# Performance work log

Measured on AMD Instinct MI355X. Metric: run time of the kernel, lower is better.

Reference implementation:

```python
import jax, jax.numpy as jnp
import numpy as np

ALPHA, BETA, LAMB, GAMMA = 1.0, 1.0, 1e-4, 1.0
K_NN, TAU = 50, 0.1
EPS = 1e-8


def _sqdist(A, B):
    # ||a - b||^2, clamped at 0 like the torch code
    d2 = (A * A).sum(1)[:, None] + (B * B).sum(1)[None, :] - 2.0 * (A @ B.T)
    return jnp.maximum(d2, 0.0)


def _mmd(s, t):
    comb = jnp.concatenate([s, t], axis=0)
    sigma_sq = jax.lax.stop_gradient(jnp.median(_sqdist(comb, comb))) / 2.0
    sigma_sq = jnp.where(sigma_sq < 1e-6, jnp.float32(1.0), sigma_sq)
    g = 1.0 / (sigma_sq + EPS)
    kxx = jnp.exp(-g * _sqdist(s, s)).mean()
    kyy = jnp.exp(-g * _sqdist(t, t)).mean()
    kxy = jnp.exp(-g * _sqdist(s, t)).mean()
    return jnp.maximum(kxx + kyy - 2.0 * kxy, 0.0)


def setup_inputs() -> dict:
    key = jax.random.key(0)
    ks = jax.random.split(key, 8)
    B, d, N, Nq, K = 256, 128, 200000, 10000, K_NN
    q_batch = jax.random.normal(ks[0], (B, d), jnp.float32)
    X = jax.random.normal(ks[1], (N, d), jnp.float32)
    W = jax.random.normal(ks[2], (d, d), jnp.float32) * (1.0 / np.sqrt(d))
    b = jnp.zeros((d,), jnp.float32)
    pre_weights = jax.random.uniform(ks[3], (Nq, K), jnp.float32)
    pre_weights = pre_weights / pre_weights.sum(1, keepdims=True)
    pre_indices = jax.random.randint(ks[4], (Nq, K), 0, N)
    q_indices = jax.random.randint(ks[5], (B,), 0, Nq)
    idx = jax.random.randint(ks[6], (B,), 0, N)
    return {"q_batch": q_batch, "X": X, "W": W, "b": b,
            "pre_weights": pre_weights, "pre_indices": pre_indices,
            "q_indices": q_indices, "idx": idx}


def reference(q_batch, X, W, b, pre_weights, pre_indices, q_indices, idx):
    Tq = q_batch @ W.T + b                                   # model(q_batch), Linear(d, d)
    # ---- MMD between mapped queries and a random database batch ----
    loss_dist = _mmd(Tq, X[idx])
    # ---- exact KNN (faiss IndexFlatL2 equivalent) on detached embeddings ----
    d2_all = _sqdist(jax.lax.stop_gradient(Tq), X)           # [B, N]
    _, post_idx = jax.lax.top_k(-d2_all, K_NN)               # [B, K] nearest neighbors
    Xn = X[post_idx]                                         # [B, K, d]
    l2 = ((Tq[:, None, :] - Xn) ** 2).sum(-1)                # [B, K] (grad flows here)
    post_w = jax.nn.softmax(-l2 / TAU, axis=1)
    # ---- union-KL, vectorized over batch (exact torch.unique semantics) ----
    pre_i = pre_indices[q_indices]                           # [B, K]
    pre_w = pre_weights[q_indices]                           # [B, K]
    cat = jnp.concatenate([pre_i, post_idx], axis=1)         # [B, 2K]
    # multiplicity of each id within the concatenated list -> collapse duplicates
    mult = (cat[:, :, None] == cat[:, None, :]).sum(-1).astype(jnp.float32)  # [B, 2K]
    p_raw = jnp.einsum('bmk,bk->bm',
                       (cat[:, :, None] == pre_i[:, None, :]).astype(jnp.float32), pre_w)
    q_raw = jnp.einsum('bmk,bk->bm',
                       (cat[:, :, None] == post_idx[:, None, :]).astype(jnp.float32), post_w)
    p_c = jnp.maximum(p_raw, EPS)
    q_c = jnp.maximum(q_raw, EPS)
    p = p_c / (p_c / mult).sum(1, keepdims=True)             # normalize over union
    q = q_c / (q_c / mult).sum(1, keepdims=True)
    kl = ((p * (jnp.log(p) - jnp.log(q))) / mult).sum(1)     # KL(p || q) per sample
    loss_knn = kl.mean()
    # ---- L2 regularization of model params & anchor loss ----
    loss_reg = 0.5 * ((W ** 2).sum() + (b ** 2).sum())
    loss_anchor = ((Tq - q_batch) ** 2).sum(1).mean()
    total = ALPHA * loss_dist + BETA * loss_knn + LAMB * loss_reg + GAMMA * loss_anchor
    return jnp.stack([total, loss_dist, loss_knn, loss_anchor])
```

## Files before the change

kernel.cpp:

```cpp
#include <hip/hip_runtime.h>
#include <cstdint>

#define D 128
#define NPTS 200000
#define KNN 50
#define CAP 8192
#define NS 8192
#define SLACK 2.0f
#define EB 2048

#define OFF_ACC    0
#define OFF_SEL    256
#define OFF_CNT    1024
#define OFF_HIST0  17408
#define OFF_HIST12 148480
#define ZERO_BYTES 214016
#define OFF_COMB   214016
#define OFF_D2     476160
#define OFF_XN     1524736
#define OFF_SAMP   2324736
#define OFF_EBUF   2324736
#define OFF_THR    10713344
#define OFF_CANDI  10714368
#define OFF_KSG    19102976
#define OFF_BCNT   19102976
#define OFF_TQSW   27491584
#define OFF_XBF    27557120
#define OFF_ANCP   78757120
#define OFF_WREGP  78758144

typedef __attribute__((ext_vector_type(8))) short bf16x8;
typedef __attribute__((ext_vector_type(4))) float f32x4;
typedef const __attribute__((address_space(1))) void* gas_p;
typedef __attribute__((address_space(3))) void* las_p;

__device__ __forceinline__ unsigned fkey(float f) {
    unsigned u = __float_as_uint(f);
    return u ^ ((unsigned)((int)u >> 31) | 0x80000000u);
}

__device__ __forceinline__ void stage8k(const unsigned short* __restrict__ g,
                                        unsigned short* l, int w, int lane)
{
    #pragma unroll
    for (int j = 0; j < 2; j++) {
        const unsigned short* gp = g + j * 2048 + w * 512 + lane * 8;
        unsigned short* lp = l + j * 2048 + w * 512;
        __builtin_amdgcn_global_load_lds((gas_p)gp, (las_p)lp, 16, 0, 0);
    }
}

__global__ void k_phase1(const float* __restrict__ q, const float* __restrict__ X,
                         const float* __restrict__ W, const float* __restrict__ bb,
                         const int* __restrict__ idx, float* __restrict__ comb,
                         unsigned short* __restrict__ tqsw, unsigned short* __restrict__ xbf,
                         float* __restrict__ xn, float* __restrict__ ancp,
                         float* __restrict__ wregp, float* __restrict__ wszero)
{
    const int blk = blockIdx.x, t = threadIdx.x;
    if (blk < 12500) {
        __shared__ float xr4[4][16];
        const int lr = t & 15;
        const float4* src = (const float4*)(X + ((long)(blk * 16 + lr)) * D + (t >> 4) * 8);
        float4 v0 = src[0], v1 = src[1];
        uint4 pk;
        pk.x = (__float_as_uint(v0.x) >> 16) | (__float_as_uint(v0.y) & 0xFFFF0000u);
        pk.y = (__float_as_uint(v0.z) >> 16) | (__float_as_uint(v0.w) & 0xFFFF0000u);
        pk.z = (__float_as_uint(v1.x) >> 16) | (__float_as_uint(v1.y) & 0xFFFF0000u);
        pk.w = (__float_as_uint(v1.z) >> 16) | (__float_as_uint(v1.w) & 0xFFFF0000u);
        *(uint4*)(xbf + (long)blk * 2048 + t * 8) = pk;
        float ssq = v0.x*v0.x + v0.y*v0.y + v0.z*v0.z + v0.w*v0.w
                  + v1.x*v1.x + v1.y*v1.y + v1.z*v1.z + v1.w*v1.w;
        ssq += __shfl_down(ssq, 32);
        ssq += __shfl_down(ssq, 16);
        if ((t & 63) < 16) xr4[t >> 6][lr] = ssq;
        __syncthreads();
        if (t < 16) xn[blk * 16 + t] = xr4[0][t] + xr4[1][t] + xr4[2][t] + xr4[3][t];
    } else if (blk < 12628) {
        __shared__ float rowv[2][D];
        __shared__ float red[2][D];
        const int half = t >> 7, tt = t & 127;
        const int row = (blk - 12500) * 2 + half;
        rowv[half][tt] = q[row * D + tt];
        __syncthreads();
        float s = 0.f;
        const float* wr = W + tt * D;
        #pragma unroll 4
        for (int k = 0; k < D; k++) s = fmaf(rowv[half][k], wr[k], s);
        s += bb[tt];
        comb[row * D + tt] = s;
        unsigned ub = __float_as_uint(s);
        unsigned short hv = (unsigned short)((ub + 0x7fffu + ((ub >> 16) & 1u)) >> 16);
        int ksb = tt >> 5, quad = (tt & 31) >> 3, jj = tt & 7;
        int lane = quad * 16 + (row & 15);
        tqsw[(row >> 4) * 2048 + ksb * 512 + lane * 8 + jj] = hv;
        float dd = s - rowv[half][tt];
        red[half][tt] = dd * dd;
        __syncthreads();
        for (int off = 64; off > 0; off >>= 1) { if (tt < off) red[half][tt] += red[half][tt + off]; __syncthreads(); }
        if (tt == 0) ancp[row] = red[half][0];
    } else if (blk < 12756) {
        const int half = t >> 7, tt = t & 127;
        const int i = (blk - 12628) * 2 + half;
        comb[(256 + i) * D + tt] = X[(long)idx[i] * D + tt];
    } else if (blk < 12760) {
        __shared__ float wred[4];
        const int base = (blk - 12756) * 4096;
        float s = 0.f;
        #pragma unroll 4
        for (int k = 0; k < 16; k++) { float v = W[base + k * 256 + t]; s = fmaf(v, v, s); }
        if (blk == 12756 && t < D) { float v = bb[t]; s = fmaf(v, v, s); }
        #pragma unroll
        for (int off = 32; off > 0; off >>= 1) s += __shfl_down(s, off);
        if ((t & 63) == 0) wred[t >> 6] = s;
        __syncthreads();
        if (t == 0) wregp[blk - 12756] = wred[0] + wred[1] + wred[2] + wred[3];
    } else {
        uint4* z = (uint4*)wszero;
        const uint4 zz = make_uint4(0u, 0u, 0u, 0u);
        for (int i = (blk - 12760) * 256 + t; i < (ZERO_BYTES / 16); i += 1024) z[i] = zz;
    }
}

__global__ void k_d2m(const float* __restrict__ comb, float* __restrict__ D2w,
                      unsigned* __restrict__ hist0, const unsigned short* __restrict__ tqsw,
                      const unsigned short* __restrict__ xbf, const float* __restrict__ xn,
                      float* __restrict__ samp)
{
    __shared__ __align__(16) char smraw[51456];
    const int b = blockIdx.x, t = threadIdx.x;
    if (b < 1024) {
        float (*cj)[D + 1] = (float(*)[D + 1])smraw;
        float (*ci)[D]     = (float(*)[D])(smraw + 33024);
        unsigned* h        = (unsigned*)(smraw + 35072);
        const int ib = b >> 3, jb = b & 7;
        const int w = t >> 6, l = t & 63;
        for (int m = t; m < 4096; m += 256) h[m] = 0;
        const int irow = ib * 4 + w;
        ci[w][l] = comb[irow * D + l];
        ci[w][l + 64] = comb[irow * D + l + 64];
        const float4* src = (const float4*)(comb + (jb * 64) * D);
        #pragma unroll
        for (int m = 0; m < 8; m++) {
            int u = m * 256 + t;
            int r = u >> 5, c = u & 31;
            float4 v = src[u];
            cj[r][c * 4 + 0] = v.x; cj[r][c * 4 + 1] = v.y; cj[r][c * 4 + 2] = v.z; cj[r][c * 4 + 3] = v.w;
        }
        __syncthreads();
        float s = 0.f;
        #pragma unroll 4
        for (int k = 0; k < D; k++) { float d = ci[w][k] - cj[l][k]; s = fmaf(d, d, s); }
        D2w[irow * 512 + jb * 64 + l] = s;
        atomicAdd(&h[__float_as_uint(s) >> 20], 1u);
        __syncthreads();
        const int sh = (ib + jb) & 7;
        for (int m = t; m < 4096; m += 256) { unsigned v = h[m]; if (v) atomicAdd(&hist0[m * 8 + sh], v); }
    } else {
        unsigned short* sb = (unsigned short*)smraw;
        const int w = t >> 6, lane = t & 63;
        const int lr = lane & 15, quad = lane >> 4;
        const int ck = b - 1024;
        stage8k(xbf + (long)ck * 4096, sb, w, lane);
        bf16x8 a[4][4];
        #pragma unroll
        for (int i = 0; i < 4; i++)
            #pragma unroll
            for (int ks = 0; ks < 4; ks++)
                a[i][ks] = *(const bf16x8*)(tqsw + (w * 4 + i) * 2048 + ks * 512 + lane * 8);
        __syncthreads();
        #pragma unroll
        for (int tt = 0; tt < 2; tt++) {
            const int r = (ck * 2 + tt) * 16 + lr;
            float xnv = xn[r];
            bf16x8 bfr[4];
            #pragma unroll
            for (int ks = 0; ks < 4; ks++)
                bfr[ks] = *(const bf16x8*)(sb + tt * 2048 + ks * 512 + lane * 8);
            f32x4 acc4[4];
            #pragma unroll
            for (int i = 0; i < 4; i++) acc4[i] = (f32x4){0.f, 0.f, 0.f, 0.f};
            #pragma unroll
            for (int ks = 0; ks < 4; ks++)
                #pragma unroll
                for (int i = 0; i < 4; i++)
                    acc4[i] = __builtin_amdgcn_mfma_f32_16x16x32_bf16(a[i][ks], bfr[ks], acc4[i], 0, 0, 0);
            #pragma unroll
            for (int i = 0; i < 4; i++)
                #pragma unroll
                for (int reg = 0; reg < 4; reg++) {
                    int qq = w * 64 + i * 16 + quad * 4 + reg;
                    samp[qq * NS + r] = xnv - 2.f * acc4[i][reg];
                }
        }
    }
}

__global__ void k_h1thr(const float* __restrict__ D2w, unsigned* __restrict__ hist12,
                        const unsigned* __restrict__ hist0, unsigned* __restrict__ sel,
                        const float* __restrict__ samp, float* __restrict__ thr)
{
    __shared__ unsigned buf[8192];
    __shared__ unsigned bins[4096];
    __shared__ unsigned part[256];
    __shared__ unsigned selll[4];
    __shared__ unsigned wred[4];
    const int t = threadIdx.x;
    if (blockIdx.x < 256) {
        unsigned s = 0;
        #pragma unroll
        for (int m = 0; m < 16; m++) {
            int bin = t * 16 + m;
            unsigned bs = 0;
            #pragma unroll
            for (int sh = 0; sh < 8; sh++) bs += hist0[bin * 8 + sh];
            bins[bin] = bs;
            s += bs;
        }
        part[t] = s;
        for (int m = t; m < 8192; m += 256) buf[m] = 0;
        __syncthreads();
        if (t == 0) {
            for (int tg = 0; tg < 2; tg++) {
                unsigned r = tg ? 131072u : 131071u;
                int c = 0;
                while (part[c] <= r) { r -= part[c]; c++; }
                int b = c * 16;
                while (bins[b] <= r) { r -= bins[b]; b++; }
                selll[2 * tg] = (unsigned)b; selll[2 * tg + 1] = r;
            }
            if (blockIdx.x == 0) {
                sel[0] = selll[0]; sel[1] = selll[1]; sel[2] = selll[2]; sel[3] = selll[3];
            }
        }
        __syncthreads();
        unsigned p0 = selll[0], p1 = selll[2];
        const int e0 = blockIdx.x * 1024;
        for (int m = 0; m < 4; m++) {
            unsigned key = __float_as_uint(D2w[e0 + m * 256 + t]);
            if ((key >> 20) == p0) atomicAdd(&buf[(key >> 8) & 0xFFFu], 1u);
            if ((key >> 20) == p1) atomicAdd(&buf[4096 + ((key >> 8) & 0xFFFu)], 1u);
        }
        __syncthreads();
        for (int m = t; m < 8192; m += 256) { unsigned v = buf[m]; if (v) atomicAdd(&hist12[m], v); }
    } else {
        const int q = blockIdx.x - 256;
        unsigned kreg[32];
        #pragma unroll
        for (int i = 0; i < 32; i++) kreg[i] = fkey(samp[q * NS + i * 256 + t]);
        unsigned v = 0;
        for (int bit = 31; bit >= 0; bit--) {
            unsigned trial = v | (1u << bit);
            unsigned c = 0;
            #pragma unroll
            for (int i = 0; i < 32; i++) c += (kreg[i] < trial) ? 1u : 0u;
            #pragma unroll
            for (int off = 32; off > 0; off >>= 1) c += __shfl_down(c, off);
            if ((t & 63) == 0) wred[t >> 6] = c;
            __syncthreads();
            unsigned total = wred[0] + wred[1] + wred[2] + wred[3];
            __syncthreads();
            if (total <= (unsigned)(KNN - 1)) v = trial;
        }
        if (t == 0) {
            unsigned orig = (v & 0x80000000u) ? (v ^ 0x80000000u) : ~v;
            thr[q] = __uint_as_float(orig) + SLACK;
        }
    }
}

__global__ __launch_bounds__(256) void k_filt2(const unsigned short* __restrict__ tqsw,
    const unsigned short* __restrict__ xbf, const float* __restrict__ xn,
    const float* __restrict__ thr, unsigned* __restrict__ ebuf, unsigned* __restrict__ bcnt,
    const float* __restrict__ D2w, unsigned* __restrict__ hist12,
    unsigned* __restrict__ sel)
{
    if (blockIdx.x >= 1024) {
        __shared__ unsigned h2c[512];
        __shared__ unsigned part2[256];
        __shared__ unsigned pfx[2];
        __shared__ unsigned rr[2];
        const int t = threadIdx.x;
        for (int tg = 0; tg < 2; tg++) {
            const unsigned* hh = hist12 + tg * 4096;
            unsigned s = 0;
            for (int m = 0; m < 16; m++) s += hh[t * 16 + m];
            part2[t] = s;
            __syncthreads();
            if (t == 0) {
                unsigned r = sel[1 + 2 * tg];
                int c = 0;
                while (part2[c] <= r) { r -= part2[c]; c++; }
                int b = c * 16;
                while (hh[b] <= r) { r -= hh[b]; b++; }
                pfx[tg] = (sel[2 * tg] << 12) | (unsigned)b;
                rr[tg] = r;
            }
            __syncthreads();
        }
        if (blockIdx.x == 1024 && t == 0) {
            sel[4] = pfx[0]; sel[5] = rr[0]; sel[6] = pfx[1]; sel[7] = rr[1];
        }
        h2c[t] = 0; h2c[256 + t] = 0;
        __syncthreads();
        unsigned p0 = pfx[0], p1 = pfx[1];
        const int e0 = (blockIdx.x - 1024) * 1024;
        for (int m = 0; m < 4; m++) {
            unsigned key = __float_as_uint(D2w[e0 + m * 256 + t]);
            if ((key >> 8) == p0) atomicAdd(&h2c[key & 0xFFu], 1u);
            if ((key >> 8) == p1) atomicAdd(&h2c[256 + (key & 0xFFu)], 1u);
        }
        __syncthreads();
        unsigned* gp = hist12 + 8192;
        unsigned v0 = h2c[t], v1 = h2c[256 + t];
        if (v0) atomicAdd(&gp[t], v0);
        if (v1) atomicAdd(&gp[4096 + t], v1);
        return;
    }
    __shared__ unsigned short sb[2][4096];
    __shared__ unsigned lbuf[1024];
    __shared__ unsigned lcnt;
    __shared__ unsigned gbase;
    const int t = threadIdx.x;
    const int w = t >> 6, lane = t & 63;
    const int lr = lane & 15, quad = lane >> 4;
    unsigned* eb = ebuf + (unsigned)blockIdx.x * EB;
    bf16x8 a[4][4];
    #pragma unroll
    for (int i = 0; i < 4; i++)
        #pragma unroll
        for (int ks = 0; ks < 4; ks++)
            a[i][ks] = *(const bf16x8*)(tqsw + (w * 4 + i) * 2048 + ks * 512 + lane * 8);
    float th_r[4][4];
    #pragma unroll
    for (int i = 0; i < 4; i++)
        #pragma unroll
        for (int reg = 0; reg < 4; reg++)
            th_r[i][reg] = thr[w * 64 + i * 16 + quad * 4 + reg];
    int ck = blockIdx.x;
    int cur = 0;
    if (t == 0) { lcnt = 0; gbase = 0; }
    stage8k(xbf + (long)ck * 4096, sb[0], w, lane);
    __syncthreads();
    while (true) {
        const int ckn = ck + 1024;
        const bool has = ckn < 6250;
        if (has) stage8k(xbf + (long)ckn * 4096, sb[cur ^ 1], w, lane);
        #pragma unroll
        for (int tt = 0; tt < 2; tt++) {
            const int r = (ck * 2 + tt) * 16 + lr;
            float xnv = xn[r];
            bf16x8 b[4];
            #pragma unroll
            for (int ks = 0; ks < 4; ks++)
                b[ks] = *(const bf16x8*)(sb[cur] + tt * 2048 + ks * 512 + lane * 8);
            f32x4 acc4[4];
            #pragma unroll
            for (int i = 0; i < 4; i++) acc4[i] = (f32x4){0.f, 0.f, 0.f, 0.f};
            #pragma unroll
            for (int ks = 0; ks < 4; ks++)
                #pragma unroll
                for (int i = 0; i < 4; i++)
                    acc4[i] = __builtin_amdgcn_mfma_f32_16x16x32_bf16(a[i][ks], b[ks], acc4[i], 0, 0, 0);
            #pragma unroll
            for (int i = 0; i < 4; i++)
                #pragma unroll
                for (int reg = 0; reg < 4; reg++) {
                    float s = xnv - 2.f * acc4[i][reg];
                    if (s <= th_r[i][reg]) {
                        unsigned qq = (unsigned)(w * 64 + i * 16 + quad * 4 + reg);
                        unsigned p = atomicAdd(&lcnt, 1u);
                        if (p < 1024u) lbuf[p] = (qq << 18) | (unsigned)r;
                        else {
                            unsigned d = gbase + p;
                            if (d < EB) eb[d] = (qq << 18) | (unsigned)r;
                        }
                    }
                }
        }
        __syncthreads();
        unsigned n = lcnt;
        if (!has || n >= 512u) {
            unsigned nf = (n < 1024u) ? n : 1024u;
            unsigned gb = gbase;
            for (unsigned m = t; m < nf; m += 256) {
                unsigned d = gb + m;
                if (d < EB) eb[d] = lbuf[m];
            }
            __syncthreads();
            if (t == 0) { gbase = gb + n; lcnt = 0; }
            __syncthreads();
        }
        if (!has) break;
        ck = ckn; cur ^= 1;
    }
    if (t == 0) bcnt[blockIdx.x] = (gbase < EB) ? gbase : EB;
}

__global__ __launch_bounds__(256) void k_scatmmd(const unsigned* __restrict__ ebuf,
    const unsigned* __restrict__ bcnt, int* __restrict__ cand_i, unsigned* __restrict__ cnt,
    const float* __restrict__ D2w, const unsigned* __restrict__ hist12,
    const unsigned* __restrict__ sel, float* __restrict__ acc)
{
    const int t = threadIdx.x;
    if (blockIdx.x >= 128) {
        __shared__ unsigned h2[512];
        __shared__ float gsh;
        __shared__ float part[12];
        const int w = t >> 6;
        h2[t] = hist12[8192 + t];
        h2[256 + t] = hist12[8192 + 4096 + t];
        __syncthreads();
        if (t == 0) {
            unsigned key[2];
            for (int tg = 0; tg < 2; tg++) {
                unsigned r = sel[5 + 2 * tg];
                const unsigned* hh = h2 + tg * 256;
                int b = 0;
                while (hh[b] <= r) { r -= hh[b]; b++; }
                key[tg] = (sel[4 + 2 * tg] << 8) | (unsigned)b;
            }
            float med = 0.5f * (__uint_as_float(key[0]) + __uint_as_float(key[1]));
            float ssq = 0.5f * med;
            if (ssq < 1e-6f) ssq = 1.0f;
            gsh = 1.0f / (ssq + 1e-8f);
        }
        __syncthreads();
        const float g = gsh;
        float s[3] = {0.f, 0.f, 0.f};
        const int e0 = (blockIdx.x - 128) * 1024;
        #pragma unroll
        for (int m = 0; m < 4; m++) {
            int e = e0 + m * 256 + t;
            int i = e >> 9, j = e & 511;
            float v = expf(-g * D2w[e]);
            int qd = (i < 256) ? ((j < 256) ? 0 : 2) : ((j < 256) ? 2 : 1);
            s[qd] += v;
        }
        #pragma unroll
        for (int c = 0; c < 3; c++) {
            float x = s[c];
            #pragma unroll
            for (int off = 32; off > 0; off >>= 1) x += __shfl_down(x, off);
            if ((t & 63) == 0) part[w * 3 + c] = x;
        }
        __syncthreads();
        if (t == 0)
            for (int c = 0; c < 3; c++)
                atomicAdd(&acc[2 + c], part[c] + part[3 + c] + part[6 + c] + part[9 + c]);
        return;
    }
    __shared__ unsigned hist[256];
    __shared__ unsigned startp[256];
    const int b0 = blockIdx.x * 8;
    hist[t] = 0;
    __syncthreads();
    for (int b = b0; b < b0 + 8; b++) {
        unsigned n = bcnt[b];
        const unsigned* e = ebuf + (unsigned)b * EB;
        for (unsigned m = t; m < n; m += 256)
            atomicAdd(&hist[e[m] >> 18], 1u);
    }
    __syncthreads();
    unsigned c = hist[t];
    if (c) {
        unsigned base = atomicAdd(&cnt[t * 16], c);
        startp[t] = ((unsigned)t << 13) + base;
    }
    __syncthreads();
    for (int b = b0; b < b0 + 8; b++) {
        unsigned n = bcnt[b];
        const unsigned* e = ebuf + (unsigned)b * EB;
        for (unsigned m = t; m < n; m += 256) {
            unsigned ent = e[m];
            unsigned qq = ent >> 18;
            unsigned pos = atomicAdd(&startp[qq], 1u);
            if (pos < ((qq + 1u) << 13)) cand_i[pos] = (int)(ent & 0x3FFFFu);
        }
    }
}

__global__ void k_rescore(const float* __restrict__ comb, const float* __restrict__ X,
                          const float* __restrict__ xn, const int* __restrict__ cand_i,
                          const unsigned* __restrict__ cnt, unsigned* __restrict__ ksg)
{
    __shared__ float qrow[D];
    const int q = blockIdx.x, sp = blockIdx.y, t = threadIdx.x;
    if (t < D) qrow[t] = comb[q * D + t];
    __syncthreads();
    unsigned nn = cnt[q * 16];
    const int n = (nn < (unsigned)CAP) ? (int)nn : CAP;
    const int g = t >> 3, j = t & 7;
    for (int m = sp * 32 + g; m < n; m += 512) {
        int r = cand_i[q * CAP + m];
        const float4* xr = (const float4*)(X + (long)r * D);
        float s = 0.f;
        #pragma unroll
        for (int p = 0; p < 4; p++) {
            float4 xv = xr[j * 4 + p];
            float4 qv = *(const float4*)&qrow[(j * 4 + p) * 4];
            s = fmaf(xv.x, qv.x, fmaf(xv.y, qv.y, fmaf(xv.z, qv.z, fmaf(xv.w, qv.w, s))));
        }
        s += __shfl_down(s, 4); s += __shfl_down(s, 2); s += __shfl_down(s, 1);
        if (j == 0) ksg[q * CAP + m] = fkey(xn[r] - 2.f * s);
    }
}

__global__ void k_post2(const float* __restrict__ comb, const float* __restrict__ X,
                        const int* __restrict__ cand_i, const unsigned* __restrict__ cnt,
                        const unsigned* __restrict__ ksg, const int* __restrict__ pri,
                        const float* __restrict__ prw, const int* __restrict__ qix,
                        float* __restrict__ acc, unsigned* __restrict__ sel,
                        const float* __restrict__ ancp, const float* __restrict__ wregp,
                        float* __restrict__ out)
{
    __shared__ unsigned ks[CAP];
    __shared__ float qrow[D];
    __shared__ unsigned wred[4];
    __shared__ unsigned wpos, eqn;
    __shared__ int eq[64];
    __shared__ int pidx[KNN];
    __shared__ float l2s[KNN];
    __shared__ float pw[KNN];
    __shared__ int ci[100];
    __shared__ float pwv[50], qwv[50];
    __shared__ float pterm[100], qterm[100], kterm[100];
    __shared__ float Sp, Sq;
    const int q = blockIdx.x, t = threadIdx.x;
    if (t < D) qrow[t] = comb[q * D + t];
    if (t == 0) { wpos = 0; eqn = 0; }
    unsigned nn = cnt[q * 16];
    const int n = (nn < (unsigned)CAP) ? (int)nn : CAP;
    for (int m = t; m < n; m += 256) ks[m] = ksg[q * CAP + m];
    __syncthreads();
    int kk = KNN - 1; if (kk > n - 1) kk = n - 1;
    unsigned v = 0;
    for (int bit = 31; bit >= 0; bit--) {
        unsigned trial = v | (1u << bit);
        unsigned c = 0;
        for (int m = t; m < n; m += 256) c += (ks[m] < trial) ? 1u : 0u;
        #pragma unroll
        for (int off = 32; off > 0; off >>= 1) c += __shfl_down(c, off);
        if ((t & 63) == 0) wred[t >> 6] = c;
        __syncthreads();
        unsigned total = wred[0] + wred[1] + wred[2] + wred[3];
        __syncthreads();
        if (total <= (unsigned)kk) v = trial;
    }
    for (int m = t; m < n; m += 256) {
        if (ks[m] < v) {
            unsigned p = atomicAdd(&wpos, 1u);
            pidx[p] = cand_i[q * CAP + m];
        } else if (ks[m] == v) {
            unsigned p = atomicAdd(&eqn, 1u);
            if (p < 64) eq[p] = cand_i[q * CAP + m];
        }
    }
    __syncthreads();
    if (t == 0) {
        int c1 = (int)wpos, need = KNN - c1;
        int ne = (eqn < 64u) ? (int)eqn : 64;
        for (int a = 0; a < ne; a++)
            for (int b2 = a + 1; b2 < ne; b2++)
                if (eq[b2] < eq[a]) { int tmp = eq[a]; eq[a] = eq[b2]; eq[b2] = tmp; }
        for (int a = 0; a < need && a < ne; a++) pidx[c1 + a] = eq[a];
    }
    __syncthreads();
    const int g = t >> 3, j = t & 7;
    for (int nb = g; nb < KNN; nb += 32) {
        long r = pidx[nb];
        const float4* xr = (const float4*)(X + r * D);
        float s = 0.f;
        #pragma unroll
        for (int p = 0; p < 4; p++) {
            float4 xv = xr[j * 4 + p];
            float4 qv = *(const float4*)&qrow[(j * 4 + p) * 4];
            float d0 = qv.x - xv.x, d1 = qv.y - xv.y, d2 = qv.z - xv.z, d3 = qv.w - xv.w;
            s += d0 * d0 + d1 * d1 + d2 * d2 + d3 * d3;
        }
        s += __shfl_down(s, 4); s += __shfl_down(s, 2); s += __shfl_down(s, 1);
        if (j == 0) l2s[nb] = s;
    }
    int qi = qix[q];
    if (t >= 128 && t < 178) { int k = t - 128; ci[k] = pri[qi * 50 + k]; pwv[k] = prw[qi * 50 + k]; }
    __syncthreads();
    if (t < 64) {
        float logit = (t < KNN) ? (-l2s[t] * 10.0f) : -3.4e38f;
        float m = logit;
        #pragma unroll
        for (int off = 32; off > 0; off >>= 1) m = fmaxf(m, __shfl_down(m, off));
        m = __shfl(m, 0);
        float e = (t < KNN) ? expf(logit - m) : 0.f;
        float ss = e;
        #pragma unroll
        for (int off = 32; off > 0; off >>= 1) ss += __shfl_down(ss, off);
        ss = __shfl(ss, 0);
        if (t < KNN) pw[t] = e / ss;
    }
    __syncthreads();
    if (t < 50) { ci[50 + t] = pidx[t]; qwv[t] = pw[t]; }
    __syncthreads();
    float pc = 0.f, qc = 0.f, mult = 0.f;
    if (t < 100) {
        int c = ci[t];
        float pr = 0.f, qr = 0.f;
        for (int k = 0; k < 50; k++) {
            bool m1 = (c == ci[k]); bool m2 = (c == ci[50 + k]);
            mult += (m1 ? 1.f : 0.f) + (m2 ? 1.f : 0.f);
            pr += m1 ? pwv[k] : 0.f;
            qr += m2 ? qwv[k] : 0.f;
        }
        pc = fmaxf(pr, 1e-8f); qc = fmaxf(qr, 1e-8f);
        pterm[t] = pc / mult; qterm[t] = qc / mult;
    }
    __syncthreads();
    if (t == 0) { float a = 0.f, b2 = 0.f; for (int m = 0; m < 100; m++) { a += pterm[m]; b2 += qterm[m]; } Sp = a; Sq = b2; }
    __syncthreads();
    if (t < 100) {
        float p = pc / Sp, qq2 = qc / Sq;
        kterm[t] = (p * (logf(p) - logf(qq2))) / mult;
    }
    __syncthreads();
    if (t == 0) {
        float s = 0.f;
        for (int m = 0; m < 100; m++) s += kterm[m];
        atomicAdd(&acc[1], s);
        __threadfence();
        unsigned old = atomicAdd(&sel[15], 1u);
        if (old == 255u) {
            __threadfence();
            float lknn = atomicAdd(&acc[1], 0.f) / 256.f;
            float reg = 0.f;
            #pragma unroll
            for (int m = 0; m < 4; m++) reg += wregp[m];
            reg *= 0.5f;
            float anc = 0.f;
            for (int m = 0; m < 256; m++) anc += ancp[m];
            float lanc = anc / 256.f;
            float kxx = acc[2] / 65536.f, kyy = acc[3] / 65536.f, kxy = acc[4] / 131072.f;
            float ld = fmaxf(kxx + kyy - 2.f * kxy, 0.f);
            out[0] = ld + lknn + 1e-4f * reg + lanc;
            out[1] = ld; out[2] = lknn; out[3] = lanc;
        }
    }
}

extern "C" void kernel_launch(void* const* d_in, const int* in_sizes, int n_in,
                              void* d_out, int out_size, void* d_ws, size_t ws_size,
                              hipStream_t stream)
{
    (void)in_sizes; (void)n_in; (void)out_size; (void)ws_size;
    const float* q   = (const float*)d_in[0];
    const float* X   = (const float*)d_in[1];
    const float* W   = (const float*)d_in[2];
    const float* bb  = (const float*)d_in[3];
    const float* prw = (const float*)d_in[4];
    const int*   pri = (const int*)d_in[5];
    const int*   qix = (const int*)d_in[6];
    const int*   idx = (const int*)d_in[7];
    float* out = (float*)d_out;
    char* ws = (char*)d_ws;
    float*    acc   = (float*)(ws + OFF_ACC);
    unsigned* sel   = (unsigned*)(ws + OFF_SEL);
    unsigned* cnt   = (unsigned*)(ws + OFF_CNT);
    unsigned* hist0 = (unsigned*)(ws + OFF_HIST0);
    unsigned* hist12= (unsigned*)(ws + OFF_HIST12);
    float*    comb  = (float*)(ws + OFF_COMB);
    float*    D2w   = (float*)(ws + OFF_D2);
    float*    xn    = (float*)(ws + OFF_XN);
    float*    samp  = (float*)(ws + OFF_SAMP);
    float*    thr   = (float*)(ws + OFF_THR);
    int*      cix   = (int*)(ws + OFF_CANDI);
    unsigned* ksg   = (unsigned*)(ws + OFF_KSG);
    unsigned* ebuf  = (unsigned*)(ws + OFF_EBUF);
    unsigned* bcnt  = (unsigned*)(ws + OFF_BCNT);
    unsigned short* tqsw = (unsigned short*)(ws + OFF_TQSW);
    unsigned short* xbf  = (unsigned short*)(ws + OFF_XBF);
    float*    ancp  = (float*)(ws + OFF_ANCP);
    float*    wregp = (float*)(ws + OFF_WREGP);

    hipLaunchKernelGGL(k_phase1,  dim3(12764),   dim3(256), 0, stream, q, X, W, bb, idx, comb, tqsw, xbf, xn, ancp, wregp, acc);
    hipLaunchKernelGGL(k_d2m,     dim3(1280),    dim3(256), 0, stream, comb, D2w, hist0, tqsw, xbf, xn, samp);
    hipLaunchKernelGGL(k_h1thr,   dim3(512),     dim3(256), 0, stream, D2w, hist12, hist0, sel, samp, thr);
    hipLaunchKernelGGL(k_filt2,   dim3(1280),    dim3(256), 0, stream, tqsw, xbf, xn, thr, ebuf, bcnt, D2w, hist12, sel);
    hipLaunchKernelGGL(k_scatmmd, dim3(384),     dim3(256), 0, stream, ebuf, bcnt, cix, cnt, D2w, hist12, sel, acc);
    hipLaunchKernelGGL(k_rescore, dim3(256, 16), dim3(256), 0, stream, comb, X, xn, cix, cnt, ksg);
    hipLaunchKernelGGL(k_post2,   dim3(256),     dim3(256), 0, stream, comb, X, cix, cnt, ksg, pri, prw, qix, acc, sel, ancp, wregp, out);
}
```

Measured before the change: 366.3 us.

## Fuse rescore into post kernel with 1024 threads and split LDS double buffer

Merges the candidate rescoring kernel into the final post-processing kernel. The fused kernel uses 1024-thread blocks and writes the rescored keys straight into shared memory instead of a global buffer, which removes one launch and the round trip of the key array. It also holds keys in registers for the radix select. The filter kernel's double buffer becomes two named LDS arrays selected by an explicit phase branch, so buffer addresses are static. The cost is that rescoring now runs on only 256 blocks instead of 4096, which reduces the parallelism available for the gather over X.

```diff
diff --git a/kernel.cpp b/kernel.cpp
--- a/kernel.cpp
+++ b/kernel.cpp
@@ -22,7 +22,6 @@
 #define OFF_EBUF   2324736
 #define OFF_THR    10713344
 #define OFF_CANDI  10714368
-#define OFF_KSG    19102976
 #define OFF_BCNT   19102976
 #define OFF_TQSW   27491584
 #define OFF_XBF    27557120
@@ -268,6 +267,42 @@
         }
     }
 }
+
+#define FILT_BODY(SBUF)                                                              \
+    do {                                                                             \
+        _Pragma("unroll")                                                            \
+        for (int tt = 0; tt < 2; tt++) {                                             \
+            const int r = (ck * 2 + tt) * 16 + lr;                                   \
+            float xnv = xn[r];                                                       \
+            bf16x8 bv[4];                                                            \
+            _Pragma("unroll")                                                        \
+            for (int ks2 = 0; ks2 < 4; ks2++)                                        \
+                bv[ks2] = *(const bf16x8*)(SBUF + tt * 2048 + ks2 * 512 + lane * 8); \
+            f32x4 acc4[4];                                                           \
+            _Pragma("unroll")                                                        \
+            for (int i = 0; i < 4; i++) acc4[i] = (f32x4){0.f, 0.f, 0.f, 0.f};       \
+            _Pragma("unroll")                                                        \
+            for (int ks2 = 0; ks2 < 4; ks2++)                                        \
+                _Pragma("unroll")                                                    \
+                for (int i = 0; i < 4; i++)                                          \
+                    acc4[i] = __builtin_amdgcn_mfma_f32_16x16x32_bf16(a[i][ks2], bv[ks2], acc4[i], 0, 0, 0); \
+            _Pragma("unroll")                                                        \
+            for (int i = 0; i < 4; i++)                                              \
+                _Pragma("unroll")                                                    \
+                for (int reg = 0; reg < 4; reg++) {                                  \
+                    float s = xnv - 2.f * acc4[i][reg];                              \
+                    if (s <= th_r[i][reg]) {                                         \
+                        unsigned qq = (unsigned)(w * 64 + i * 16 + quad * 4 + reg);  \
+                        unsigned p = atomicAdd(&lcnt, 1u);                           \
+                        if (p < 1024u) lbuf[p] = (qq << 18) | (unsigned)r;           \
+                        else {                                                       \
+                            unsigned dd2 = gbase + p;                                \
+                            if (dd2 < EB) eb[dd2] = (qq << 18) | (unsigned)r;        \
+                        }                                                            \
+                    }                                                                \
+                }                                                                    \
+        }                                                                            \
+    } while (0)
 
 __global__ __launch_bounds__(256) void k_filt2(const unsigned short* __restrict__ tqsw,
     const unsigned short* __restrict__ xbf, const float* __restrict__ xn,
@@ -317,7 +352,8 @@
         if (v1) atomicAdd(&gp[4096 + t], v1);
         return;
     }
-    __shared__ unsigned short sb[2][4096];
+    __shared__ unsigned short sbA[4096];
+    __shared__ unsigned short sbB[4096];
     __shared__ unsigned lbuf[1024];
     __shared__ unsigned lcnt;
     __shared__ unsigned gbase;
@@ -338,45 +374,19 @@
         for (int reg = 0; reg < 4; reg++)
             th_r[i][reg] = thr[w * 64 + i * 16 + quad * 4 + reg];
     int ck = blockIdx.x;
-    int cur = 0;
+    bool phaseA = true;
     if (t == 0) { lcnt = 0; gbase = 0; }
-    stage8k(xbf + (long)ck * 4096, sb[0], w, lane);
+    stage8k(xbf + (long)ck * 4096, sbA, w, lane);
     __syncthreads();
     while (true) {
         const int ckn = ck + 1024;
         const bool has = ckn < 6250;
-        if (has) stage8k(xbf + (long)ckn * 4096, sb[cur ^ 1], w, lane);
-        #pragma unroll
-        for (int tt = 0; tt < 2; tt++) {
-            const int r = (ck * 2 + tt) * 16 + lr;
-            float xnv = xn[r];
-            bf16x8 b[4];
-            #pragma unroll
-            for (int ks = 0; ks < 4; ks++)
-                b[ks] = *(const bf16x8*)(sb[cur] + tt * 2048 + ks * 512 + lane * 8);
-            f32x4 acc4[4];
-            #pragma unroll
-            for (int i = 0; i < 4; i++) acc4[i] = (f32x4){0.f, 0.f, 0.f, 0.f};
-            #pragma unroll
-            for (int ks = 0; ks < 4; ks++)
-                #pragma unroll
-                for (int i = 0; i < 4; i++)
-                    acc4[i] = __builtin_amdgcn_mfma_f32_16x16x32_bf16(a[i][ks], b[ks], acc4[i], 0, 0, 0);
-            #pragma unroll
-            for (int i = 0; i < 4; i++)
-                #pragma unroll
-                for (int reg = 0; reg < 4; reg++) {
-                    float s = xnv - 2.f * acc4[i][reg];
-                    if (s <= th_r[i][reg]) {
-                        unsigned qq = (unsigned)(w * 64 + i * 16 + quad * 4 + reg);
-                        unsigned p = atomicAdd(&lcnt, 1u);
-                        if (p < 1024u) lbuf[p] = (qq << 18) | (unsigned)r;
-                        else {
-                            unsigned d = gbase + p;
-                            if (d < EB) eb[d] = (qq << 18) | (unsigned)r;
-                        }
-                    }
-                }
+        if (phaseA) {
+            if (has) stage8k(xbf + (long)ckn * 4096, sbB, w, lane);
+            FILT_BODY(sbA);
+        } else {
+            if (has) stage8k(xbf + (long)ckn * 4096, sbA, w, lane);
+            FILT_BODY(sbB);
         }
         __syncthreads();
         unsigned n = lcnt;
@@ -392,7 +402,7 @@
             __syncthreads();
         }
         if (!has) break;
-        ck = ckn; cur ^= 1;
+        ck = ckn; phaseA = !phaseA;
     }
     if (t == 0) bcnt[blockIdx.x] = (gbase < EB) ? gbase : EB;
 }
@@ -480,43 +490,19 @@
     }
 }
 
-__global__ void k_rescore(const float* __restrict__ comb, const float* __restrict__ X,
-                          const float* __restrict__ xn, const int* __restrict__ cand_i,
-                          const unsigned* __restrict__ cnt, unsigned* __restrict__ ksg)
-{
-    __shared__ float qrow[D];
-    const int q = blockIdx.x, sp = blockIdx.y, t = threadIdx.x;
-    if (t < D) qrow[t] = comb[q * D + t];
-    __syncthreads();
-    unsigned nn = cnt[q * 16];
-    const int n = (nn < (unsigned)CAP) ? (int)nn : CAP;
-    const int g = t >> 3, j = t & 7;
-    for (int m = sp * 32 + g; m < n; m += 512) {
-        int r = cand_i[q * CAP + m];
-        const float4* xr = (const float4*)(X + (long)r * D);
-        float s = 0.f;
-        #pragma unroll
-        for (int p = 0; p < 4; p++) {
-            float4 xv = xr[j * 4 + p];
-            float4 qv = *(const float4*)&qrow[(j * 4 + p) * 4];
-            s = fmaf(xv.x, qv.x, fmaf(xv.y, qv.y, fmaf(xv.z, qv.z, fmaf(xv.w, qv.w, s))));
-        }
-        s += __shfl_down(s, 4); s += __shfl_down(s, 2); s += __shfl_down(s, 1);
-        if (j == 0) ksg[q * CAP + m] = fkey(xn[r] - 2.f * s);
-    }
-}
-
-__global__ void k_post2(const float* __restrict__ comb, const float* __restrict__ X,
+__global__ __launch_bounds__(1024) void k_rp(const float* __restrict__ comb,
+                        const float* __restrict__ X,
                         const int* __restrict__ cand_i, const unsigned* __restrict__ cnt,
-                        const unsigned* __restrict__ ksg, const int* __restrict__ pri,
+                        const int* __restrict__ pri,
                         const float* __restrict__ prw, const int* __restrict__ qix,
+                        const float* __restrict__ xn,
                         float* __restrict__ acc, unsigned* __restrict__ sel,
                         const float* __restrict__ ancp, const float* __restrict__ wregp,
                         float* __restrict__ out)
 {
     __shared__ unsigned ks[CAP];
     __shared__ float qrow[D];
-    __shared__ unsigned wred[4];
+    __shared__ unsigned wred[16];
     __shared__ unsigned wpos, eqn;
     __shared__ int eq[64];
     __shared__ int pidx[KNN];
@@ -531,23 +517,46 @@
     if (t == 0) { wpos = 0; eqn = 0; }
     unsigned nn = cnt[q * 16];
     const int n = (nn < (unsigned)CAP) ? (int)nn : CAP;
-    for (int m = t; m < n; m += 256) ks[m] = ksg[q * CAP + m];
-    __syncthreads();
+    __syncthreads();
+    const int g = t >> 3, j = t & 7;
+    for (int m = g; m < n; m += 128) {
+        int r = cand_i[q * CAP + m];
+        const float4* xr = (const float4*)(X + (long)r * D);
+        float s = 0.f;
+        #pragma unroll
+        for (int p = 0; p < 4; p++) {
+            float4 xv = xr[j * 4 + p];
+            float4 qv = *(const float4*)&qrow[(j * 4 + p) * 4];
+            s = fmaf(xv.x, qv.x, fmaf(xv.y, qv.y, fmaf(xv.z, qv.z, fmaf(xv.w, qv.w, s))));
+        }
+        s += __shfl_down(s, 4); s += __shfl_down(s, 2); s += __shfl_down(s, 1);
+        if (j == 0) ks[m] = fkey(xn[r] - 2.f * s);
+    }
+    __syncthreads();
+    unsigned kreg[8];
+    #pragma unroll
+    for (int i = 0; i < 8; i++) {
+        int m = i * 1024 + t;
+        kreg[i] = (m < n) ? ks[m] : 0xFFFFFFFFu;
+    }
     int kk = KNN - 1; if (kk > n - 1) kk = n - 1;
     unsigned v = 0;
     for (int bit = 31; bit >= 0; bit--) {
         unsigned trial = v | (1u << bit);
         unsigned c = 0;
-        for (int m = t; m < n; m += 256) c += (ks[m] < trial) ? 1u : 0u;
+        #pragma unroll
+        for (int i = 0; i < 8; i++) c += (kreg[i] < trial) ? 1u : 0u;
         #pragma unroll
         for (int off = 32; off > 0; off >>= 1) c += __shfl_down(c, off);
         if ((t & 63) == 0) wred[t >> 6] = c;
         __syncthreads();
-        unsigned total = wred[0] + wred[1] + wred[2] + wred[3];
+        unsigned total = 0;
+        #pragma unroll
+        for (int i = 0; i < 16; i++) total += wred[i];
         __syncthreads();
         if (total <= (unsigned)kk) v = trial;
     }
-    for (int m = t; m < n; m += 256) {
+    for (int m = t; m < n; m += 1024) {
         if (ks[m] < v) {
             unsigned p = atomicAdd(&wpos, 1u);
             pidx[p] = cand_i[q * CAP + m];
@@ -566,8 +575,7 @@
         for (int a = 0; a < need && a < ne; a++) pidx[c1 + a] = eq[a];
     }
     __syncthreads();
-    const int g = t >> 3, j = t & 7;
-    for (int nb = g; nb < KNN; nb += 32) {
+    for (int nb = g; nb < KNN; nb += 128) {
         long r = pidx[nb];
         const float4* xr = (const float4*)(X + r * D);
         float s = 0.f;
@@ -671,7 +679,6 @@
     float*    samp  = (float*)(ws + OFF_SAMP);
     float*    thr   = (float*)(ws + OFF_THR);
     int*      cix   = (int*)(ws + OFF_CANDI);
-    unsigned* ksg   = (unsigned*)(ws + OFF_KSG);
     unsigned* ebuf  = (unsigned*)(ws + OFF_EBUF);
     unsigned* bcnt  = (unsigned*)(ws + OFF_BCNT);
     unsigned short* tqsw = (unsigned short*)(ws + OFF_TQSW);
@@ -684,6 +691,5 @@
     hipLaunchKernelGGL(k_h1thr,   dim3(512),     dim3(256), 0, stream, D2w, hist12, hist0, sel, samp, thr);
     hipLaunchKernelGGL(k_filt2,   dim3(1280),    dim3(256), 0, stream, tqsw, xbf, xn, thr, ebuf, bcnt, D2w, hist12, sel);
     hipLaunchKernelGGL(k_scatmmd, dim3(384),     dim3(256), 0, stream, ebuf, bcnt, cix, cnt, D2w, hist12, sel, acc);
-    hipLaunchKernelGGL(k_rescore, dim3(256, 16), dim3(256), 0, stream, comb, X, xn, cix, cnt, ksg);
-    hipLaunchKernelGGL(k_post2,   dim3(256),     dim3(256), 0, stream, comb, X, cix, cnt, ksg, pri, prw, qix, acc, sel, ancp, wregp, out);
-}
+    hipLaunchKernelGGL(k_rp,      dim3(256),     dim3(1024), 0, stream, comb, X, cix, cnt, pri, prw, qix, xn, acc, sel, ancp, wregp, out);
+}
```

After: 358.9 us. 2.0% less time.
